# Kernel tuning notes

Measured on AMD Instinct MI355X. Metric: run time of the kernel, lower is better.

Reference implementation:

```python
import jax, jax.numpy as jnp
import numpy as np

B, N = 8, 2048
IN_F, MID1, HID, MID2, OUT_F = 128, 128, 128, 128, 128
BIG = 9e15  # matches torch's 9000000000000000.0 additive mask constant


def _linear_params(key, out_d, in_d):
    # torch Linear layout: W is [out, in]
    kw, kb = jax.random.split(key)
    w = jax.random.normal(kw, (out_d, in_d), jnp.float32) * (1.0 / np.sqrt(in_d))
    b = jax.random.normal(kb, (out_d,), jnp.float32) * 0.01
    return w, b


def setup_inputs() -> dict:
    key = jax.random.key(0)
    ks = jax.random.split(key, 16)
    h = jax.random.normal(ks[0], (B, N, IN_F), jnp.float32)
    adj = jax.random.randint(ks[1], (B, N, N), 0, 2).astype(jnp.float32)
    vae2_fetures = jax.random.normal(ks[2], (B, N, OUT_F), jnp.float32)
    Wv1, bv1 = _linear_params(ks[3], MID1, IN_F)
    Wk1, bk1 = _linear_params(ks[4], MID1, IN_F)
    Wq1, bq1 = _linear_params(ks[5], MID1, IN_F)
    Wo1, bo1 = _linear_params(ks[6], HID, MID1)
    Wv2, bv2 = _linear_params(ks[7], MID2, HID)
    Wk2, bk2 = _linear_params(ks[8], MID2, HID)
    Wq2, bq2 = _linear_params(ks[9], MID2, HID)
    Wo2, bo2 = _linear_params(ks[10], OUT_F, MID2)
    Wf, bf = _linear_params(ks[11], OUT_F, 2 * OUT_F)
    return {
        "h": h, "adj": adj, "vae2_fetures": vae2_fetures,
        "Wv1": Wv1, "bv1": bv1, "Wk1": Wk1, "bk1": bk1, "Wq1": Wq1, "bq1": bq1,
        "Wo1": Wo1, "bo1": bo1,
        "Wv2": Wv2, "bv2": bv2, "Wk2": Wk2, "bk2": bk2, "Wq2": Wq2, "bq2": bq2,
        "Wo2": Wo2, "bo2": bo2, "Wf": Wf, "bf": bf,
    }


def _lin(x, W, b):
    return jnp.einsum('bnd,od->bno', x, W) + b


def _masked_att_block(x, adj, Wq, bq, Wk, bk, Wv, bv):
    v = jax.nn.relu(_lin(x, Wv, bv))          # [B,N,D]
    q = jax.nn.relu(_lin(x, Wq, bq))          # [B,N,D]
    k = jax.nn.relu(_lin(x, Wk, bk))          # [B,N,D]
    s = jnp.einsum('bnd,bmd->bnm', q, k)       # [B,N,N]
    masked = s * adj - BIG * (1.0 - adj)       # multiplicative + additive mask
    att = jax.nn.softmax(masked, axis=-1)
    return jnp.einsum('bnm,bmd->bnd', att, v)


def reference(h, adj, vae2_fetures,
              Wv1, bv1, Wk1, bk1, Wq1, bq1, Wo1, bo1,
              Wv2, bv2, Wk2, bk2, Wq2, bq2, Wo2, bo2,
              Wf, bf):
    f1 = _masked_att_block(h, adj, Wq1, bq1, Wk1, bk1, Wv1, bv1)
    f1 = _lin(f1, Wo1, bo1)                    # [B,N,HID]
    f2 = _masked_att_block(f1, adj, Wq2, bq2, Wk2, bk2, Wv2, bv2)
    f2 = _lin(f2, Wo2, bo2)                    # [B,N,OUT_F]
    f3 = jnp.concatenate([f2, vae2_fetures], axis=2)
    return _lin(f3, Wf, bf)                    # [B,N,OUT_F]
```

## Files before the change

### kernel.cpp

```cpp
#include <hip/hip_runtime.h>

typedef short s16x8 __attribute__((ext_vector_type(8)));
typedef float f32x4 __attribute__((ext_vector_type(4)));
typedef unsigned short u16x4v __attribute__((ext_vector_type(4)));

#define NSPLIT 4
#define NROWS 16384
#define MSHIFT 44.0f

__device__ __forceinline__ unsigned short f2bf(float f) {
  union { float fl; unsigned int i; } v; v.fl = f;
  unsigned int x = v.i;
  x += 0x7fffu + ((x >> 16) & 1u);
  return (unsigned short)(x >> 16);
}
__device__ __forceinline__ s16x8 load8_bf16(const unsigned short* p) {
  return *(const s16x8*)p;
}
__device__ __forceinline__ s16x8 load8_f32(const float* p) {
  float4 a = *(const float4*)p;
  float4 b = *(const float4*)(p + 4);
  s16x8 r;
  r[0] = (short)f2bf(a.x); r[1] = (short)f2bf(a.y);
  r[2] = (short)f2bf(a.z); r[3] = (short)f2bf(a.w);
  r[4] = (short)f2bf(b.x); r[5] = (short)f2bf(b.y);
  r[6] = (short)f2bf(b.z); r[7] = (short)f2bf(b.w);
  return r;
}
__device__ __forceinline__ int vperm(int nn) {
  return (nn & ~31) | (((nn >> 2) & 3) << 3) | (((nn >> 4) & 1) << 2);
}

__global__ __launch_bounds__(256) void pack_kernel(
    const float4* __restrict__ adj4, unsigned long long* __restrict__ mask)
{
  const int lane = threadIdx.x & 63;
  const size_t nvec = (size_t)NROWS * 2048 / 4;
  const size_t stride = (size_t)gridDim.x * 256;
  for (size_t i = (size_t)blockIdx.x * 256 + threadIdx.x; i < nvec; i += stride) {
    float4 v = adj4[i];
    unsigned long long n = (v.x != 0.f ? 1u : 0u) | (v.y != 0.f ? 2u : 0u) |
                           (v.z != 0.f ? 4u : 0u) | (v.w != 0.f ? 8u : 0u);
    unsigned long long word = n << (4 * (lane & 15));
    word |= __shfl_xor(word, 1, 64);
    word |= __shfl_xor(word, 2, 64);
    word |= __shfl_xor(word, 4, 64);
    word |= __shfl_xor(word, 8, 64);
    if ((lane & 15) == 0) mask[(i * 4) >> 6] = word;
  }
}

template <int MODE>
__device__ __forceinline__ void qkv_body(
    const float* __restrict__ X, const float* __restrict__ W,
    const float* __restrict__ bias, unsigned short* __restrict__ out)
{
  const int t = threadIdx.x;
  const int w = t >> 6;
  const int lane = t & 63;
  const int l15 = lane & 15;
  const int quad = lane >> 4;
  const int mbase = blockIdx.x * 16;

  s16x8 a[4];
  const float* ar = X + (size_t)(mbase + l15) * 128;
#pragma unroll
  for (int ks = 0; ks < 4; ++ks) a[ks] = load8_f32(ar + ks * 32 + quad * 8);

#pragma unroll
  for (int nt = 0; nt < 2; ++nt) {
    const int n = (w * 2 + nt) * 16 + l15;
    f32x4 acc = {0.f, 0.f, 0.f, 0.f};
    const float* wr = W + (size_t)n * 128;
#pragma unroll
    for (int ks = 0; ks < 4; ++ks)
      acc = __builtin_amdgcn_mfma_f32_16x16x32_bf16(
          a[ks], load8_f32(wr + ks * 32 + quad * 8), acc, 0, 0, 0);
    const float bv = bias[n];
    if (MODE == 0) {
#pragma unroll
      for (int r = 0; r < 4; ++r)
        out[(size_t)(mbase + quad * 4 + r) * 128 + n] = f2bf(fmaxf(acc[r] + bv, 0.f));
    } else {
      const int b  = mbase >> 11;
      const int nn = (mbase & 2047) + quad * 4;
      u16x4v pk;
#pragma unroll
      for (int r = 0; r < 4; ++r) pk[r] = f2bf(fmaxf(acc[r] + bv, 0.f));
      *(u16x4v*)(out + (size_t)(b * 128 + n) * 2048 + vperm(nn)) = pk;
    }
  }
}

__global__ __launch_bounds__(256) void qkv1_kernel(
    const float* __restrict__ x,
    const float* __restrict__ Wq, const float* __restrict__ bq, unsigned short* __restrict__ oq,
    const float* __restrict__ Wk, const float* __restrict__ bk, unsigned short* __restrict__ ok,
    const float* __restrict__ Wv, const float* __restrict__ bv, unsigned short* __restrict__ ovt)
{
  if (blockIdx.y == 0)      qkv_body<0>(x, Wq, bq, oq);
  else if (blockIdx.y == 1) qkv_body<0>(x, Wk, bk, ok);
  else                      qkv_body<1>(x, Wv, bv, ovt);
}

__global__ __launch_bounds__(256, 2) void attn_kernel(
    const unsigned short* __restrict__ Q,
    const unsigned short* __restrict__ K,
    const unsigned short* __restrict__ VT,
    const unsigned long long* __restrict__ MASK,
    float* __restrict__ pO, float* __restrict__ pl)
{
  __shared__ __align__(16) unsigned short kbuf[64][136];
  __shared__ __align__(16) unsigned short vbuf[128][72];

  const int t = threadIdx.x;
  const int w = t >> 6;
  const int lane = t & 63;
  const int l15 = lane & 15;
  const int quad = lane >> 4;

  const int gq0 = blockIdx.x * 128;
  const int b   = gq0 >> 11;
  const int q0  = gq0 & 2047;
  const int wq0 = q0 + w * 32;
  const int kc0 = blockIdx.y * (2048 / NSPLIT);

  const unsigned short* Kb  = K  + (size_t)(b * 2048) * 128;
  const unsigned short* VTb = VT + (size_t)(b * 128) * 2048;
  const unsigned long long* Mb = MASK + (size_t)b * 2048 * 32;

  s16x8 qf[2][4];
#pragma unroll
  for (int mt = 0; mt < 2; ++mt) {
    const unsigned short* qrow = Q + (size_t)(gq0 + w * 32 + mt * 16 + l15) * 128;
#pragma unroll
    for (int ks = 0; ks < 4; ++ks) qf[mt][ks] = load8_bf16(qrow + ks * 32 + quad * 8);
  }

  s16x8 ones;
#pragma unroll
  for (int i = 0; i < 8; ++i) ones[i] = (short)0x3F80;

  f32x4 accO[2][8];
  f32x4 accL[2];
#pragma unroll
  for (int mt = 0; mt < 2; ++mt) {
    accL[mt] = (f32x4){0.f, 0.f, 0.f, 0.f};
#pragma unroll
    for (int dt = 0; dt < 8; ++dt) accO[mt][dt] = (f32x4){0.f, 0.f, 0.f, 0.f};
  }

  s16x8 kr[4], vr[4];
#pragma unroll
  for (int i = 0; i < 4; ++i) {
    int slot = i * 256 + t;
    kr[i] = load8_bf16(Kb + (size_t)(kc0 + (slot >> 4)) * 128 + (slot & 15) * 8);
    vr[i] = load8_bf16(VTb + (size_t)(slot >> 3) * 2048 + kc0 + (slot & 7) * 8);
  }

  for (int kc = kc0; kc < kc0 + 2048 / NSPLIT; kc += 64) {
    __syncthreads();
#pragma unroll
    for (int i = 0; i < 4; ++i) {
      int slot = i * 256 + t;
      *(s16x8*)&kbuf[slot >> 4][(slot & 15) * 8] = kr[i];
      *(s16x8*)&vbuf[slot >> 3][(slot & 7) * 8]  = vr[i];
    }
    __syncthreads();

    unsigned long long mw[2];
#pragma unroll
    for (int mt = 0; mt < 2; ++mt)
      mw[mt] = Mb[(size_t)(wq0 + mt * 16 + l15) * 32 + (kc >> 6)];

    if (kc + 64 < kc0 + 2048 / NSPLIT) {
#pragma unroll
      for (int i = 0; i < 4; ++i) {
        int slot = i * 256 + t;
        kr[i] = load8_bf16(Kb + (size_t)(kc + 64 + (slot >> 4)) * 128 + (slot & 15) * 8);
        vr[i] = load8_bf16(VTb + (size_t)(slot >> 3) * 2048 + (kc + 64) + (slot & 7) * 8);
      }
    }

    f32x4 sv[2][4];
#pragma unroll
    for (int nt = 0; nt < 4; ++nt) {
      sv[0][nt] = (f32x4){0.f, 0.f, 0.f, 0.f};
      sv[1][nt] = (f32x4){0.f, 0.f, 0.f, 0.f};
#pragma unroll
      for (int ks = 0; ks < 4; ++ks) {
        s16x8 kf = *(const s16x8*)&kbuf[nt * 16 + l15][ks * 32 + quad * 8];
        sv[0][nt] = __builtin_amdgcn_mfma_f32_16x16x32_bf16(kf, qf[0][ks], sv[0][nt], 0, 0, 0);
        sv[1][nt] = __builtin_amdgcn_mfma_f32_16x16x32_bf16(kf, qf[1][ks], sv[1][nt], 0, 0, 0);
      }
    }

    float p[2][4][4];
#pragma unroll
    for (int mt = 0; mt < 2; ++mt)
#pragma unroll
      for (int nt = 0; nt < 4; ++nt)
#pragma unroll
        for (int r = 0; r < 4; ++r) {
          float e = __expf(sv[mt][nt][r] - MSHIFT);
          p[mt][nt][r] = ((mw[mt] >> (nt * 16 + quad * 4 + r)) & 1ull) ? e : 0.f;
        }

    s16x8 pf[2][2];
#pragma unroll
    for (int mt = 0; mt < 2; ++mt)
#pragma unroll
      for (int ks = 0; ks < 2; ++ks) {
        s16x8 v;
#pragma unroll
        for (int j = 0; j < 4; ++j) {
          v[j]     = (short)f2bf(p[mt][2 * ks][j]);
          v[j + 4] = (short)f2bf(p[mt][2 * ks + 1][j]);
        }
        pf[mt][ks] = v;
      }

#pragma unroll
    for (int mt = 0; mt < 2; ++mt)
#pragma unroll
      for (int ks = 0; ks < 2; ++ks)
        accL[mt] = __builtin_amdgcn_mfma_f32_16x16x32_bf16(ones, pf[mt][ks], accL[mt], 0, 0, 0);

#pragma unroll
    for (int dt = 0; dt < 8; ++dt) {
#pragma unroll
      for (int ks = 0; ks < 2; ++ks) {
        s16x8 vf = *(const s16x8*)&vbuf[dt * 16 + l15][ks * 32 + quad * 8];
        accO[0][dt] = __builtin_amdgcn_mfma_f32_16x16x32_bf16(vf, pf[0][ks], accO[0][dt], 0, 0, 0);
        accO[1][dt] = __builtin_amdgcn_mfma_f32_16x16x32_bf16(vf, pf[1][ks], accO[1][dt], 0, 0, 0);
      }
    }
  }

  float* pOs = pO + (size_t)blockIdx.y * NROWS * 128;
#pragma unroll
  for (int mt = 0; mt < 2; ++mt) {
    const int qg = gq0 + w * 32 + mt * 16 + l15;
#pragma unroll
    for (int dt = 0; dt < 8; ++dt)
      *(f32x4*)(pOs + (size_t)qg * 128 + dt * 16 + quad * 4) = accO[mt][dt];
  }
  if (quad == 0) {
#pragma unroll
    for (int mt = 0; mt < 2; ++mt)
      pl[blockIdx.y * NROWS + gq0 + w * 32 + mt * 16 + l15] = accL[mt][0];
  }
}

__device__ __forceinline__ void combine_splits(
    const float* __restrict__ pO, const float* __restrict__ pl, int grow0,
    unsigned short (*At)[136])
{
  const int t = threadIdx.x;
  const int row = t >> 4;
  const int col8 = (t & 15) * 8;
  const int grow = grow0 + row;
  float lsum = 0.f;
#pragma unroll
  for (int s = 0; s < NSPLIT; ++s) lsum += pl[s * NROWS + grow];
  const float inv = (lsum > 0.f) ? 1.f / lsum : 0.f;
  float acc8[8];
#pragma unroll
  for (int i = 0; i < 8; ++i) acc8[i] = 0.f;
#pragma unroll
  for (int s = 0; s < NSPLIT; ++s) {
    const float* p = pO + (size_t)s * NROWS * 128 + (size_t)grow * 128 + col8;
    float4 x0 = *(const float4*)p;
    float4 x1 = *(const float4*)(p + 4);
    acc8[0] += x0.x; acc8[1] += x0.y; acc8[2] += x0.z; acc8[3] += x0.w;
    acc8[4] += x1.x; acc8[5] += x1.y; acc8[6] += x1.z; acc8[7] += x1.w;
  }
#pragma unroll
  for (int i = 0; i < 8; ++i) At[row][col8 + i] = f2bf(acc8[i] * inv);
}

__global__ __launch_bounds__(256) void redqkv_kernel(
    const float* __restrict__ pO, const float* __restrict__ pl,
    const float* __restrict__ Wo, const float* __restrict__ bo,
    const float* __restrict__ Wq, const float* __restrict__ bq, unsigned short* __restrict__ oq,
    const float* __restrict__ Wk, const float* __restrict__ bk, unsigned short* __restrict__ ok,
    const float* __restrict__ Wv, const float* __restrict__ bv, unsigned short* __restrict__ ovt)
{
  __shared__ __align__(16) unsigned short At[16][136];
  __shared__ __align__(16) unsigned short Bt[16][136];
  const int t = threadIdx.x;
  const int grow0 = blockIdx.x * 16;

  combine_splits(pO, pl, grow0, At);
  __syncthreads();

  const int w = t >> 6;
  const int lane = t & 63;
  const int l15 = lane & 15;
  const int quad = lane >> 4;

  s16x8 a[4];
#pragma unroll
  for (int ks = 0; ks < 4; ++ks) a[ks] = *(const s16x8*)&At[l15][ks * 32 + quad * 8];
#pragma unroll
  for (int nt = 0; nt < 2; ++nt) {
    const int n = (w * 2 + nt) * 16 + l15;
    f32x4 acc = {0.f, 0.f, 0.f, 0.f};
    const float* wr = Wo + (size_t)n * 128;
#pragma unroll
    for (int ks = 0; ks < 4; ++ks)
      acc = __builtin_amdgcn_mfma_f32_16x16x32_bf16(
          a[ks], load8_f32(wr + ks * 32 + quad * 8), acc, 0, 0, 0);
    const float bv_ = bo[n];
#pragma unroll
    for (int r = 0; r < 4; ++r) Bt[quad * 4 + r][n] = f2bf(acc[r] + bv_);
  }
  __syncthreads();

  s16x8 a2[4];
#pragma unroll
  for (int ks = 0; ks < 4; ++ks) a2[ks] = *(const s16x8*)&Bt[l15][ks * 32 + quad * 8];

#pragma unroll
  for (int which = 0; which < 3; ++which) {
    const float* W = (which == 0) ? Wq : (which == 1) ? Wk : Wv;
    const float* bb = (which == 0) ? bq : (which == 1) ? bk : bv;
    unsigned short* out = (which == 0) ? oq : (which == 1) ? ok : ovt;
#pragma unroll
    for (int nt = 0; nt < 2; ++nt) {
      const int n = (w * 2 + nt) * 16 + l15;
      f32x4 acc = {0.f, 0.f, 0.f, 0.f};
      const float* wr = W + (size_t)n * 128;
#pragma unroll
      for (int ks = 0; ks < 4; ++ks)
        acc = __builtin_amdgcn_mfma_f32_16x16x32_bf16(
            a2[ks], load8_f32(wr + ks * 32 + quad * 8), acc, 0, 0, 0);
      const float bv_ = bb[n];
      if (which < 2) {
#pragma unroll
        for (int r = 0; r < 4; ++r)
          out[(size_t)(grow0 + quad * 4 + r) * 128 + n] = f2bf(fmaxf(acc[r] + bv_, 0.f));
      } else {
        const int b  = grow0 >> 11;
        const int nn = (grow0 & 2047) + quad * 4;
        u16x4v pk;
#pragma unroll
        for (int r = 0; r < 4; ++r) pk[r] = f2bf(fmaxf(acc[r] + bv_, 0.f));
        *(u16x4v*)(out + (size_t)(b * 128 + n) * 2048 + vperm(nn)) = pk;
      }
    }
  }
}

__global__ __launch_bounds__(256) void redfinal_kernel(
    const float* __restrict__ pO, const float* __restrict__ pl,
    const float* __restrict__ Wo, const float* __restrict__ bo,
    const float* __restrict__ Wf, const float* __restrict__ bff,
    const float* __restrict__ vae2, float* __restrict__ out)
{
  __shared__ __align__(16) unsigned short At[16][136];
  __shared__ __align__(16) unsigned short Bt[16][136];
  const int t = threadIdx.x;
  const int grow0 = blockIdx.x * 16;

  combine_splits(pO, pl, grow0, At);
  __syncthreads();

  const int w = t >> 6;
  const int lane = t & 63;
  const int l15 = lane & 15;
  const int quad = lane >> 4;

  s16x8 a[4];
#pragma unroll
  for (int ks = 0; ks < 4; ++ks) a[ks] = *(const s16x8*)&At[l15][ks * 32 + quad * 8];
#pragma unroll
  for (int nt = 0; nt < 2; ++nt) {
    const int n = (w * 2 + nt) * 16 + l15;
    f32x4 acc = {0.f, 0.f, 0.f, 0.f};
    const float* wr = Wo + (size_t)n * 128;
#pragma unroll
    for (int ks = 0; ks < 4; ++ks)
      acc = __builtin_amdgcn_mfma_f32_16x16x32_bf16(
          a[ks], load8_f32(wr + ks * 32 + quad * 8), acc, 0, 0, 0);
    const float bv_ = bo[n];
#pragma unroll
    for (int r = 0; r < 4; ++r) Bt[quad * 4 + r][n] = f2bf(acc[r] + bv_);
  }
  __syncthreads();

  s16x8 a1[4], a2[4];
#pragma unroll
  for (int ks = 0; ks < 4; ++ks) a1[ks] = *(const s16x8*)&Bt[l15][ks * 32 + quad * 8];
  const float* vrow = vae2 + (size_t)(grow0 + l15) * 128;
#pragma unroll
  for (int ks = 0; ks < 4; ++ks) a2[ks] = load8_f32(vrow + ks * 32 + quad * 8);
#pragma unroll
  for (int nt = 0; nt < 2; ++nt) {
    const int n = (w * 2 + nt) * 16 + l15;
    f32x4 acc = {0.f, 0.f, 0.f, 0.f};
    const float* wr = Wf + (size_t)n * 256;
#pragma unroll
    for (int ks = 0; ks < 4; ++ks)
      acc = __builtin_amdgcn_mfma_f32_16x16x32_bf16(
          a1[ks], load8_f32(wr + ks * 32 + quad * 8), acc, 0, 0, 0);
#pragma unroll
    for (int ks = 0; ks < 4; ++ks)
      acc = __builtin_amdgcn_mfma_f32_16x16x32_bf16(
          a2[ks], load8_f32(wr + 128 + ks * 32 + quad * 8), acc, 0, 0, 0);
    const float bv_ = bff[n];
#pragma unroll
    for (int r = 0; r < 4; ++r)
      out[(size_t)(grow0 + quad * 4 + r) * 128 + n] = acc[r] + bv_;
  }
}

extern "C" void kernel_launch(void* const* d_in, const int* in_sizes, int n_in,
                              void* d_out, int out_size, void* d_ws, size_t ws_size,
                              hipStream_t stream)
{
  const float* h    = (const float*)d_in[0];
  const float* adj  = (const float*)d_in[1];
  const float* vae2 = (const float*)d_in[2];
  const float* Wv1  = (const float*)d_in[3];
  const float* bv1  = (const float*)d_in[4];
  const float* Wk1  = (const float*)d_in[5];
  const float* bk1  = (const float*)d_in[6];
  const float* Wq1  = (const float*)d_in[7];
  const float* bq1  = (const float*)d_in[8];
  const float* Wo1  = (const float*)d_in[9];
  const float* bo1  = (const float*)d_in[10];
  const float* Wv2  = (const float*)d_in[11];
  const float* bv2  = (const float*)d_in[12];
  const float* Wk2  = (const float*)d_in[13];
  const float* bk2  = (const float*)d_in[14];
  const float* Wq2  = (const float*)d_in[15];
  const float* bq2  = (const float*)d_in[16];
  const float* Wo2  = (const float*)d_in[17];
  const float* bo2  = (const float*)d_in[18];
  const float* Wf   = (const float*)d_in[19];
  const float* bff  = (const float*)d_in[20];

  char* wsb = (char*)d_ws;
  const size_t MB = 1u << 20;
  unsigned short* s_q  = (unsigned short*)(wsb + 0 * MB);
  unsigned short* s_k  = (unsigned short*)(wsb + 4 * MB);
  unsigned short* s_vt = (unsigned short*)(wsb + 8 * MB);
  unsigned long long* maskp = (unsigned long long*)(wsb + 12 * MB);
  float* pO = (float*)(wsb + 16 * MB);
  float* pl = (float*)(wsb + 48 * MB);

  pack_kernel<<<dim3(4096), dim3(256), 0, stream>>>((const float4*)adj, maskp);
  qkv1_kernel<<<dim3(1024, 3), dim3(256), 0, stream>>>(
      h, Wq1, bq1, s_q, Wk1, bk1, s_k, Wv1, bv1, s_vt);
  attn_kernel<<<dim3(128, NSPLIT), dim3(256), 0, stream>>>(
      s_q, s_k, s_vt, maskp, pO, pl);
  redqkv_kernel<<<dim3(1024), dim3(256), 0, stream>>>(
      pO, pl, Wo1, bo1, Wq2, bq2, s_q, Wk2, bk2, s_k, Wv2, bv2, s_vt);
  attn_kernel<<<dim3(128, NSPLIT), dim3(256), 0, stream>>>(
      s_q, s_k, s_vt, maskp, pO, pl);
  redfinal_kernel<<<dim3(1024), dim3(256), 0, stream>>>(
      pO, pl, Wo2, bo2, Wf, bff, vae2, (float*)d_out);
}
```

Before: 405.2 us.

## Fuse adjacency bitmask packing into first attention kernel

After: 393.0 us, median of 2. 3.0% less time.

```diff
diff --git a/kernel.cpp b/kernel.cpp
--- a/kernel.cpp
+++ b/kernel.cpp
@@ -31,25 +31,6 @@
   return (nn & ~31) | (((nn >> 2) & 3) << 3) | (((nn >> 4) & 1) << 2);
 }
 
-__global__ __launch_bounds__(256) void pack_kernel(
-    const float4* __restrict__ adj4, unsigned long long* __restrict__ mask)
-{
-  const int lane = threadIdx.x & 63;
-  const size_t nvec = (size_t)NROWS * 2048 / 4;
-  const size_t stride = (size_t)gridDim.x * 256;
-  for (size_t i = (size_t)blockIdx.x * 256 + threadIdx.x; i < nvec; i += stride) {
-    float4 v = adj4[i];
-    unsigned long long n = (v.x != 0.f ? 1u : 0u) | (v.y != 0.f ? 2u : 0u) |
-                           (v.z != 0.f ? 4u : 0u) | (v.w != 0.f ? 8u : 0u);
-    unsigned long long word = n << (4 * (lane & 15));
-    word |= __shfl_xor(word, 1, 64);
-    word |= __shfl_xor(word, 2, 64);
-    word |= __shfl_xor(word, 4, 64);
-    word |= __shfl_xor(word, 8, 64);
-    if ((lane & 15) == 0) mask[(i * 4) >> 6] = word;
-  }
-}
-
 template <int MODE>
 __device__ __forceinline__ void qkv_body(
     const float* __restrict__ X, const float* __restrict__ W,
@@ -103,11 +84,13 @@
   else                      qkv_body<1>(x, Wv, bv, ovt);
 }
 
+template <bool PACK>
 __global__ __launch_bounds__(256, 2) void attn_kernel(
     const unsigned short* __restrict__ Q,
     const unsigned short* __restrict__ K,
     const unsigned short* __restrict__ VT,
-    const unsigned long long* __restrict__ MASK,
+    const float* __restrict__ ADJ,
+    unsigned long long* __restrict__ MASK,
     float* __restrict__ pO, float* __restrict__ pl)
 {
   __shared__ __align__(16) unsigned short kbuf[64][136];
@@ -127,7 +110,8 @@
 
   const unsigned short* Kb  = K  + (size_t)(b * 2048) * 128;
   const unsigned short* VTb = VT + (size_t)(b * 128) * 2048;
-  const unsigned long long* Mb = MASK + (size_t)b * 2048 * 32;
+  const float* ADJb = ADJ + (size_t)b * 2048 * 2048;
+  unsigned long long* Mb = MASK + (size_t)b * 2048 * 32;
 
   s16x8 qf[2][4];
 #pragma unroll
@@ -169,9 +153,19 @@
     __syncthreads();
 
     unsigned long long mw[2];
-#pragma unroll
-    for (int mt = 0; mt < 2; ++mt)
-      mw[mt] = Mb[(size_t)(wq0 + mt * 16 + l15) * 32 + (kc >> 6)];
+    float4 a4[2][4];
+    if (PACK) {
+#pragma unroll
+      for (int mt = 0; mt < 2; ++mt)
+#pragma unroll
+        for (int nt = 0; nt < 4; ++nt)
+          a4[mt][nt] = *(const float4*)(
+              ADJb + (size_t)(wq0 + mt * 16 + l15) * 2048 + kc + nt * 16 + quad * 4);
+    } else {
+#pragma unroll
+      for (int mt = 0; mt < 2; ++mt)
+        mw[mt] = Mb[(size_t)(wq0 + mt * 16 + l15) * 32 + (kc >> 6)];
+    }
 
     if (kc + 64 < kc0 + 2048 / NSPLIT) {
 #pragma unroll
@@ -196,15 +190,40 @@
     }
 
     float p[2][4][4];
-#pragma unroll
-    for (int mt = 0; mt < 2; ++mt)
-#pragma unroll
-      for (int nt = 0; nt < 4; ++nt)
-#pragma unroll
-        for (int r = 0; r < 4; ++r) {
-          float e = __expf(sv[mt][nt][r] - MSHIFT);
-          p[mt][nt][r] = ((mw[mt] >> (nt * 16 + quad * 4 + r)) & 1ull) ? e : 0.f;
+    if (PACK) {
+#pragma unroll
+      for (int mt = 0; mt < 2; ++mt) {
+        unsigned long long word = 0;
+#pragma unroll
+        for (int nt = 0; nt < 4; ++nt) {
+          unsigned int nib = 0;
+#pragma unroll
+          for (int r = 0; r < 4; ++r) {
+            float av = (r == 0) ? a4[mt][nt].x : (r == 1) ? a4[mt][nt].y
+                     : (r == 2) ? a4[mt][nt].z : a4[mt][nt].w;
+            bool keep = (av != 0.f);
+            float e = __expf(sv[mt][nt][r] - MSHIFT);
+            p[mt][nt][r] = keep ? e : 0.f;
+            nib |= (keep ? 1u : 0u) << r;
+          }
+          word |= (unsigned long long)nib << (nt * 16 + quad * 4);
         }
+        word |= __shfl_xor(word, 16, 64);
+        word |= __shfl_xor(word, 32, 64);
+        if (quad == 0)
+          Mb[(size_t)(wq0 + mt * 16 + l15) * 32 + (kc >> 6)] = word;
+      }
+    } else {
+#pragma unroll
+      for (int mt = 0; mt < 2; ++mt)
+#pragma unroll
+        for (int nt = 0; nt < 4; ++nt)
+#pragma unroll
+          for (int r = 0; r < 4; ++r) {
+            float e = __expf(sv[mt][nt][r] - MSHIFT);
+            p[mt][nt][r] = ((mw[mt] >> (nt * 16 + quad * 4 + r)) & 1ull) ? e : 0.f;
+          }
+    }
 
     s16x8 pf[2][2];
 #pragma unroll
@@ -450,15 +469,14 @@
   float* pO = (float*)(wsb + 16 * MB);
   float* pl = (float*)(wsb + 48 * MB);
 
-  pack_kernel<<<dim3(4096), dim3(256), 0, stream>>>((const float4*)adj, maskp);
   qkv1_kernel<<<dim3(1024, 3), dim3(256), 0, stream>>>(
       h, Wq1, bq1, s_q, Wk1, bk1, s_k, Wv1, bv1, s_vt);
-  attn_kernel<<<dim3(128, NSPLIT), dim3(256), 0, stream>>>(
-      s_q, s_k, s_vt, maskp, pO, pl);
+  attn_kernel<true><<<dim3(128, NSPLIT), dim3(256), 0, stream>>>(
+      s_q, s_k, s_vt, adj, maskp, pO, pl);
   redqkv_kernel<<<dim3(1024), dim3(256), 0, stream>>>(
       pO, pl, Wo1, bo1, Wq2, bq2, s_q, Wk2, bk2, s_k, Wv2, bv2, s_vt);
-  attn_kernel<<<dim3(128, NSPLIT), dim3(256), 0, stream>>>(
-      s_q, s_k, s_vt, maskp, pO, pl);
+  attn_kernel<false><<<dim3(128, NSPLIT), dim3(256), 0, stream>>>(
+      s_q, s_k, s_vt, nullptr, maskp, pO, pl);
   redfinal_kernel<<<dim3(1024), dim3(256), 0, stream>>>(
       pO, pl, Wo2, bo2, Wf, bff, vae2, (float*)d_out);
 }
```
